# Optimization experiments

Hardware: AMD Instinct MI355X
Metric: run time of the kernel (lower is better)

Reference implementation:

```python
import jax, jax.numpy as jnp
import numpy as np

L, B, CIN, H, W = 32, 4, 3, 16, 16
D, HEADS, DK, DEPTH = 64, 4, 16, 2
EPS = 1e-5
BN_INV = float(1.0 / np.sqrt(1.0 + EPS))  # eval-mode BatchNorm with default stats/affine


def conv2d(x, w, b=None, pad=1, groups=1):
    y = jax.lax.conv_general_dilated(
        x, w, window_strides=(1, 1), padding=[(pad, pad), (pad, pad)],
        dimension_numbers=('NCHW', 'OIHW', 'NCHW'), feature_group_count=groups)
    if b is not None:
        y = y + b[None, :, None, None]
    return y


def layer_norm(x, w, b):
    # LayerNorm over last 3 dims [D,H,W] of (L,B,D,H,W)
    mu = jnp.mean(x, axis=(-3, -2, -1), keepdims=True)
    var = jnp.var(x, axis=(-3, -2, -1), keepdims=True)
    return (x - mu) * jax.lax.rsqrt(var + EPS) * w + b


def pos_table():
    pos = jnp.arange(L, dtype=jnp.float32)
    exp = (2.0 * (jnp.arange(D) // 2).astype(jnp.float32)) / D
    angle = pos[:, None] / jnp.power(10000.0, exp)[None, :]  # (L, D)
    # source applies sin to even POSITIONS and cos to odd POSITIONS (table[0::2]=sin)
    tab = jnp.where((jnp.arange(L) % 2 == 0)[:, None], jnp.sin(angle), jnp.cos(angle))
    return tab[:, None, :, None, None]  # (L,1,D,1,1) broadcast over B,H,W


def reference(x, gw1, gb1, gw2, gb2, gw3, gb3, gw4, gb4,
              conv1_w, conv1_b, conv2_w, conv2_b, wq, wk, wv, w0,
              ln1_w, ln1_b, ln2_w, ln2_b, ff_w1, ff_b1, ff_w2, ff_b2):
    lrelu = lambda v: jax.nn.leaky_relu(v, 0.01)
    h = x.reshape(L * B, CIN, H, W)
    for w_, b_ in ((gw1, gb1), (gw2, gb2), (gw3, gb3), (gw4, gb4)):
        h = lrelu(conv2d(h, w_, b_) * BN_INV)
    xlb = h.reshape(L, B, D, H, W) + pos_table()

    for i in range(DEPTH):
        # ---- multi-head conv attention (dec=True) ----
        y = layer_norm(xlb, ln1_w[i], ln1_b[i])
        xa = jnp.transpose(y, (1, 2, 3, 4, 0))  # (B,D,H,W,L)
        # conv1 is a 1x1 conv == pointwise linear over channels, per head
        qkv = jnp.einsum('bchwl,noc->bnohwl', xa, conv1_w[i]) \
            + conv1_b[i][None, :, :, None, None, None]  # (B,HEADS,3D,H,W,L)
        q, k, v = jnp.split(qkv, 3, axis=2)  # each (B,HEADS,D,H,W,L)
        q = jnp.einsum('bnchwl,nck->bnkhwl', q, wq[i])  # (B,HEADS,DK,H,W,L)
        k = jnp.einsum('bnchwl,nck->bnkhwl', k, wk[i])
        v = jnp.einsum('bnchwl,nck->bnkhwl', v, wv[i])

        def head_conv(t):
            # 5x5 conv per head (no bias): conv2(Q_i + K_j) = conv_w(Q)_i + conv_w(K)_j + bias
            z = jnp.transpose(t, (0, 5, 1, 2, 3, 4)).reshape(B * L, HEADS * DK, H, W)
            z = conv2d(z, conv2_w[i].reshape(HEADS * DK, DK, 5, 5), None, pad=2, groups=HEADS)
            return jnp.transpose(z.reshape(B, L, HEADS, DK, H, W), (0, 2, 3, 4, 5, 1))

        cq = head_conv(q)
        ck = head_conv(k)
        logits = cq[..., :, None] + ck[..., None, :] \
            + conv2_b[i][None, :, :, None, None, None, None]  # (B,HEADS,DK,H,W,Lq,Lk)
        a = jax.nn.softmax(logits, axis=-1)
        vout = jnp.einsum('bnkhwij,bnkhwj->bnkhwi', a, v)   # (B,HEADS,DK,H,W,L)
        vcat = vout.reshape(B, D, H, W, L)                  # concat heads on channel dim
        attn = jnp.einsum('bchwl,co->bohwl', vcat, w0[i])
        xlb = xlb + jnp.transpose(attn, (4, 0, 1, 2, 3))

        # ---- feed-forward over the TIME dimension (Linear on L) ----
        y = layer_norm(xlb, ln2_w[i], ln2_b[i])
        xp = jnp.transpose(y, (1, 2, 3, 4, 0))  # (B,D,H,W,L)
        h1 = lrelu(jnp.einsum('bchwl,ml->bchwm', xp, ff_w1[i]) + ff_b1[i])
        ff = jnp.einsum('bchwm,lm->bchwl', h1, ff_w2[i]) + ff_b2[i]
        xlb = xlb + jnp.transpose(ff, (4, 0, 1, 2, 3))
    return xlb


def setup_inputs() -> dict:
    key = jax.random.key(0)
    specs = {
        'x': (L, B, CIN, H, W),
        'gw1': (4, 3, 3, 3), 'gb1': (4,), 'gw2': (6, 4, 3, 3), 'gb2': (6,),
        'gw3': (8, 6, 3, 3), 'gb3': (8,), 'gw4': (64, 8, 3, 3), 'gb4': (64,),
        'conv1_w': (DEPTH, HEADS, 3 * D, D), 'conv1_b': (DEPTH, HEADS, 3 * D),
        'conv2_w': (DEPTH, HEADS, DK, DK, 5, 5), 'conv2_b': (DEPTH, HEADS, DK),
        'wq': (DEPTH, HEADS, D, DK), 'wk': (DEPTH, HEADS, D, DK), 'wv': (DEPTH, HEADS, D, DK),
        'w0': (DEPTH, D, D),
        'ln1_w': (DEPTH, D, H, W), 'ln1_b': (DEPTH, D, H, W),
        'ln2_w': (DEPTH, D, H, W), 'ln2_b': (DEPTH, D, H, W),
        'ff_w1': (DEPTH, 4 * L, L), 'ff_b1': (DEPTH, 4 * L),
        'ff_w2': (DEPTH, L, 4 * L), 'ff_b2': (DEPTH, L),
    }
    out = {}
    for idx, (name, shape) in enumerate(specs.items()):
        g = jax.random.normal(jax.random.fold_in(key, idx), shape, dtype=jnp.float32)
        if name == 'x':
            out[name] = g
        elif name in ('ln1_w', 'ln2_w'):
            out[name] = 1.0 + 0.05 * g
        else:
            out[name] = 0.05 * g
    return out
```

## Files before the change

kernel.cpp:

```cpp
#include <hip/hip_runtime.h>
#include <math.h>

#define LL 32
#define BB 4
#define DD 64
#define NH 4
#define DKK 16
#define BN_INV 0.9999950000374997f

__device__ __forceinline__ float lrelu(float v){ return v > 0.f ? v : 0.01f*v; }

__global__ __launch_bounds__(256) void k_prep(
    const float* __restrict__ c1w, const float* __restrict__ c1b,
    const float* __restrict__ wk,  const float* __restrict__ wv,
    const float* __restrict__ w2,  const float* __restrict__ gw4,
    const float* __restrict__ ffw2,
    float* __restrict__ A, float* __restrict__ bf, float* __restrict__ pos,
    float* __restrict__ wT, float* __restrict__ wT3, float* __restrict__ w2T){
  int blk = blockIdx.x, t = threadIdx.x;
  if(blk < 64){
    int tid = blk*256 + t;
    int k = tid & 15, d = (tid>>4)&63, n=(tid>>10)&3, tt=(tid>>12)&1, i=tid>>13;
    const float* wsel = (tt ? wv : wk) + (i*NH+n)*64*16;
    const float* cw   = c1w + ((i*NH+n)*192 + (tt+1)*64)*64;
    float acc = 0.f;
    for(int c=0;c<64;++c) acc += cw[c*64+d]*wsel[c*16+k];
    A[tid] = acc;
    if(d==0){
      const float* cb = c1b + (i*NH+n)*192 + (tt+1)*64;
      float ba=0.f;
      for(int c=0;c<64;++c) ba += cb[c]*wsel[c*16+k];
      bf[((i*2+tt)*4+n)*16+k] = ba;
    }
  } else if(blk < 72){
    int tid = (blk-64)*256 + t;
    int d = tid & 63, l = tid >> 6;
    float ex = (float)(d>>1) / 32.0f;
    float angle = (float)l * powf(10000.0f, -ex);
    pos[tid] = (l & 1) ? cosf(angle) : sinf(angle);
  } else if(blk < 272){
    int tid = (blk-72)*256 + t;
    int k = tid & 15; int rest = tid >> 4;
    int tap = rest % 25; int rest2 = rest / 25;
    int c = rest2 & 15; int dn = rest2 >> 4;
    wT[tid] = w2[((dn*16 + k)*16 + c)*25 + tap];
  } else if(blk < 290){
    int tid = (blk-272)*256 + t;
    int co = tid & 63, ct = tid >> 6;
    wT3[ct*64 + co] = gw4[co*72 + ct];
  } else {
    int tid = (blk-290)*256 + t;
    int l = tid & 31; int m = (tid>>5)&127; int dep = tid>>12;
    w2T[tid] = ffw2[dep*4096 + l*128 + m];
  }
}

__global__ __launch_bounds__(256) void k_front(const float* __restrict__ x,
    const float* __restrict__ gw1, const float* __restrict__ gb1,
    const float* __restrict__ gw2, const float* __restrict__ gb2,
    const float* __restrict__ gw3, const float* __restrict__ gb3,
    float* __restrict__ out8){
  __shared__ float sh[4212];
  float* T0 = sh; float* T1 = sh + 972; float* T2 = sh + 2268;
  int f = blockIdx.x, t = threadIdx.x;
  int h = t>>4, w = t&15;
  for(int j=t;j<4212;j+=256) sh[j]=0.f;
  __syncthreads();
  for(int ci=0;ci<3;++ci) T0[ci*324 + (h+1)*18 + (w+1)] = x[f*768 + ci*256 + t];
  __syncthreads();
  for(int co=0;co<4;++co){
    float acc = gb1[co];
    for(int ci=0;ci<3;++ci){
      const float* tb = T0 + ci*324 + h*18 + w;
      const float* wb = gw1 + co*27 + ci*9;
      #pragma unroll
      for(int dy=0;dy<3;++dy)
        #pragma unroll
        for(int dx=0;dx<3;++dx) acc += tb[dy*18+dx]*wb[dy*3+dx];
    }
    T1[co*324 + (h+1)*18 + (w+1)] = lrelu(acc*BN_INV);
  }
  __syncthreads();
  for(int co=0;co<6;++co){
    float acc = gb2[co];
    for(int ci=0;ci<4;++ci){
      const float* tb = T1 + ci*324 + h*18 + w;
      const float* wb = gw2 + co*36 + ci*9;
      #pragma unroll
      for(int dy=0;dy<3;++dy)
        #pragma unroll
        for(int dx=0;dx<3;++dx) acc += tb[dy*18+dx]*wb[dy*3+dx];
    }
    T2[co*324 + (h+1)*18 + (w+1)] = lrelu(acc*BN_INV);
  }
  __syncthreads();
  for(int co=0;co<8;++co){
    float acc = gb3[co];
    for(int ci=0;ci<6;++ci){
      const float* tb = T2 + ci*324 + h*18 + w;
      const float* wb = gw3 + co*54 + ci*9;
      #pragma unroll
      for(int dy=0;dy<3;++dy)
        #pragma unroll
        for(int dx=0;dx<3;++dx) acc += tb[dy*18+dx]*wb[dy*3+dx];
    }
    out8[f*2048 + co*256 + t] = lrelu(acc*BN_INV);
  }
}

__global__ __launch_bounds__(256) void k_conv3_l4(const float* __restrict__ in8,
    const float* __restrict__ wT3, const float* __restrict__ gb4,
    const float* __restrict__ pos, float* __restrict__ out){
  __shared__ float tile[8*324];
  __shared__ float wsl[1152];
  int blk = blockIdx.x; int g = blk & 3; int f = blk >> 2;
  int t = threadIdx.x; int h = t>>4, w = t&15;
  for(int j=t;j<2592;j+=256) tile[j]=0.f;
  for(int j=t;j<1152;j+=256){
    int ct = j>>4, c16 = j&15;
    wsl[j] = wT3[ct*64 + g*16 + c16];
  }
  __syncthreads();
  for(int ci=0;ci<8;++ci) tile[ci*324 + (h+1)*18 + (w+1)] = in8[f*2048 + ci*256 + t];
  __syncthreads();
  float acc[16];
  #pragma unroll
  for(int q=0;q<16;++q) acc[q] = gb4[g*16+q];
  for(int ci=0;ci<8;++ci){
    const float* tb = tile + ci*324 + h*18 + w;
    #pragma unroll
    for(int dy=0;dy<3;++dy){
      #pragma unroll
      for(int dx=0;dx<3;++dx){
        float v = tb[dy*18+dx];
        const float* wp = wsl + (ci*9+dy*3+dx)*16;
        float4 wa = *(const float4*)(wp);
        float4 wb = *(const float4*)(wp+4);
        float4 wc = *(const float4*)(wp+8);
        float4 wd = *(const float4*)(wp+12);
        acc[0]+=v*wa.x; acc[1]+=v*wa.y; acc[2]+=v*wa.z; acc[3]+=v*wa.w;
        acc[4]+=v*wb.x; acc[5]+=v*wb.y; acc[6]+=v*wb.z; acc[7]+=v*wb.w;
        acc[8]+=v*wc.x; acc[9]+=v*wc.y; acc[10]+=v*wc.z; acc[11]+=v*wc.w;
        acc[12]+=v*wd.x; acc[13]+=v*wd.y; acc[14]+=v*wd.z; acc[15]+=v*wd.w;
      }
    }
  }
  int l = f >> 2;
  #pragma unroll
  for(int q=0;q<16;++q){
    float r = lrelu(acc[q]*BN_INV) + pos[l*64 + g*16 + q];
    out[f*16384 + (g*16+q)*256 + t] = r;
  }
}

__global__ __launch_bounds__(1024) void k_stats(const float* __restrict__ x,
                                                float* __restrict__ stats){
  int g = blockIdx.x, t = threadIdx.x;
  const float4* xb = (const float4*)(x + g*16384);
  float s=0.f, s2=0.f;
  #pragma unroll
  for(int j=0;j<4;++j){
    float4 v = xb[t + j*1024];
    s  += v.x + v.y + v.z + v.w;
    s2 += v.x*v.x + v.y*v.y + v.z*v.z + v.w*v.w;
  }
  __shared__ float ls[1024], ls2[1024];
  ls[t]=s; ls2[t]=s2; __syncthreads();
  for(int off=512;off>0;off>>=1){
    if(t<off){ ls[t]+=ls[t+off]; ls2[t]+=ls2[t+off]; }
    __syncthreads();
  }
  if(t==0){
    float mu  = ls[0]*(1.0f/16384.f);
    float var = ls2[0]*(1.0f/16384.f) - mu*mu;
    stats[g*2]   = mu;
    stats[g*2+1] = rsqrtf(var + 1e-5f);
  }
}

__global__ __launch_bounds__(256) void k_kv(const float* __restrict__ x,
                     const float* __restrict__ lnw, const float* __restrict__ lnb,
                     const float* __restrict__ stats,
                     const float* __restrict__ A, const float* __restrict__ bf,
                     float* __restrict__ K, float* __restrict__ V, int dep){
  int blk = blockIdx.x;
  int n = blk & 3; int lb = blk >> 2;
  int t = threadIdx.x;
  float mu = stats[lb*2], ri = stats[lb*2+1];
  const float* xb  = x   + lb*16384 + t;
  const float* wbp = lnw + t;
  const float* bbp = lnb + t;
  const float* akb = A + ((dep*2+0)*4+n)*1024;
  const float* avb = A + ((dep*2+1)*4+n)*1024;
  float kacc[16], vacc[16];
  #pragma unroll
  for(int q=0;q<16;++q){
    kacc[q] = bf[((dep*2+0)*4+n)*16+q];
    vacc[q] = bf[((dep*2+1)*4+n)*16+q];
  }
  for(int d=0;d<64;++d){
    float yv = (xb[d*256]-mu)*ri*wbp[d*256] + bbp[d*256];
    const float* ak = akb + d*16;
    const float* av = avb + d*16;
    #pragma unroll
    for(int q=0;q<16;++q){ kacc[q] += yv*ak[q]; vacc[q] += yv*av[q]; }
  }
  int l = lb >> 2, b = lb & 3;
  int base = ((b*32+l)*4+n)*4096 + t;
  #pragma unroll
  for(int q=0;q<16;++q){ K[base + q*256] = kacc[q]; V[base + q*256] = vacc[q]; }
}

__global__ __launch_bounds__(256) void k_conv5(const float* __restrict__ K,
                       const float* __restrict__ wT, float* __restrict__ CK, int dep){
  __shared__ float tile[16*400];
  int blk = blockIdx.x;
  int khalf = blk & 1; int fh = blk >> 1; int n = fh & 3;
  int t = threadIdx.x;
  const float* kb = K + fh*4096;
  for(int j=t;j<6400;j+=256) tile[j]=0.f;
  __syncthreads();
  int h = t>>4, w = t&15;
  for(int c=0;c<16;++c) tile[c*400 + (h+2)*20 + (w+2)] = kb[c*256+t];
  __syncthreads();
  const float* wb = wT + (dep*4+n)*6400 + khalf*8;
  float acc[8] = {0.f,0.f,0.f,0.f,0.f,0.f,0.f,0.f};
  for(int c=0;c<16;++c){
    const float* tb = tile + c*400 + h*20 + w;
    const float* wc = wb + c*400;
    #pragma unroll
    for(int dy=0;dy<5;++dy){
      #pragma unroll
      for(int dx=0;dx<5;++dx){
        float v = tb[dy*20+dx];
        const float* wp = wc + (dy*5+dx)*16;
        float4 wa = *(const float4*)(wp);
        float4 wbv = *(const float4*)(wp+4);
        acc[0]+=v*wa.x; acc[1]+=v*wa.y; acc[2]+=v*wa.z; acc[3]+=v*wa.w;
        acc[4]+=v*wbv.x; acc[5]+=v*wbv.y; acc[6]+=v*wbv.z; acc[7]+=v*wbv.w;
      }
    }
  }
  float* ob = CK + fh*4096 + khalf*8*256;
  #pragma unroll
  for(int q=0;q<8;++q) ob[q*256+t] = acc[q];
}

__global__ void k_soft(const float* __restrict__ CK, const float* __restrict__ V,
                       float* __restrict__ vout){
  int idx = blockIdx.x*256 + threadIdx.x;
  int p = idx&255; int k=(idx>>8)&15; int n=(idx>>12)&3; int b=idx>>14;
  int base = (b*128 + n)*4096 + k*256 + p;
  float e[32]; float m = -1e30f;
  for(int l=0;l<32;++l){ float v = CK[base + l*16384]; e[l]=v; m = fmaxf(m,v); }
  float s = 0.f;
  for(int l=0;l<32;++l){ e[l] = expf(e[l]-m); s += e[l]; }
  float inv = 1.f/s, acc = 0.f;
  for(int l=0;l<32;++l) acc += e[l]*V[base + l*16384];
  vout[((b*4+n)*16+k)*256+p] = acc*inv;
}

__global__ void k_w0res(const float* __restrict__ vout, const float* __restrict__ w0,
                        float* __restrict__ xlb, int dep){
  int idx = blockIdx.x*256 + threadIdx.x;
  int p = idx&255; int o=(idx>>8)&63; int b=idx>>14;
  const float* vb = vout + b*64*256 + p;
  const float* wb = w0 + dep*4096 + o;
  float acc = 0.f;
  for(int c=0;c<64;++c) acc += vb[c*256]*wb[c*64];
  for(int l=0;l<32;++l) xlb[((l*4+b)*64+o)*256 + p] += acc;
}

__global__ __launch_bounds__(256) void k_ff(float* __restrict__ xlb,
                     const float* __restrict__ lnw, const float* __restrict__ lnb,
                     const float* __restrict__ stats,
                     const float* __restrict__ w1, const float* __restrict__ b1,
                     const float* __restrict__ w2T, const float* __restrict__ b2,
                     int dep){
  __shared__ float pfa[4*2048];
  int t = threadIdx.x;
  int lane = t & 63;
  int w = __builtin_amdgcn_readfirstlane(t >> 6);
  int blk = blockIdx.x;
  int elem = blk*64 + lane;
  int b = elem >> 14;
  int e = elem & 16383;
  float lw  = lnw[e];
  float lbv = lnb[e];
  float xv[32], yv[32];
  #pragma unroll
  for(int l=0;l<32;++l) xv[l] = xlb[elem + l*65536];
  #pragma unroll
  for(int l=0;l<32;++l){
    float mu = stats[(l*4+b)*2];
    float ri = stats[(l*4+b)*2+1];
    yv[l] = (xv[l]-mu)*ri*lw + lbv;
  }
  float fa[32];
  if(w==0){
    #pragma unroll
    for(int l=0;l<32;++l) fa[l] = b2[dep*32+l];
  } else {
    #pragma unroll
    for(int l=0;l<32;++l) fa[l] = 0.f;
  }
  const float* w1b  = w1  + dep*4096 + w*1024;
  const float* w2Tb = w2T + dep*4096 + w*1024;
  const float* b1b  = b1  + dep*128  + w*32;
  #pragma unroll 4
  for(int mm=0;mm<32;++mm){
    float s0=0.f,s1=0.f,s2=0.f,s3=0.f;
    #pragma unroll
    for(int l=0;l<32;l+=4){
      s0 += yv[l+0]*w1b[mm*32+l+0];
      s1 += yv[l+1]*w1b[mm*32+l+1];
      s2 += yv[l+2]*w1b[mm*32+l+2];
      s3 += yv[l+3]*w1b[mm*32+l+3];
    }
    float s = lrelu(((s0+s1)+(s2+s3)) + b1b[mm]);
    #pragma unroll
    for(int l=0;l<32;++l) fa[l] += s*w2Tb[mm*32+l];
  }
  #pragma unroll
  for(int l=0;l<32;++l) pfa[w*2048 + l*64 + lane] = fa[l];
  __syncthreads();
  #pragma unroll
  for(int j=0;j<8;++j){
    int pi = t + j*256;
    float sum = pfa[pi] + pfa[pi+2048] + pfa[pi+4096] + pfa[pi+6144];
    int l = pi >> 6;
    xlb[blk*64 + lane + l*65536] = xv[l] + sum;
  }
}

extern "C" void kernel_launch(void* const* d_in, const int* in_sizes, int n_in,
                              void* d_out, int out_size, void* d_ws, size_t ws_size,
                              hipStream_t stream) {
  const float* x       = (const float*)d_in[0];
  const float* gw1     = (const float*)d_in[1];
  const float* gb1     = (const float*)d_in[2];
  const float* gw2     = (const float*)d_in[3];
  const float* gb2     = (const float*)d_in[4];
  const float* gw3     = (const float*)d_in[5];
  const float* gb3     = (const float*)d_in[6];
  const float* gw4     = (const float*)d_in[7];
  const float* gb4     = (const float*)d_in[8];
  const float* conv1_w = (const float*)d_in[9];
  const float* conv1_b = (const float*)d_in[10];
  const float* conv2_w = (const float*)d_in[11];
  const float* wk      = (const float*)d_in[14];
  const float* wv      = (const float*)d_in[15];
  const float* w0      = (const float*)d_in[16];
  const float* ln1_w   = (const float*)d_in[17];
  const float* ln1_b   = (const float*)d_in[18];
  const float* ln2_w   = (const float*)d_in[19];
  const float* ln2_b   = (const float*)d_in[20];
  const float* ff_w1   = (const float*)d_in[21];
  const float* ff_b1   = (const float*)d_in[22];
  const float* ff_w2   = (const float*)d_in[23];
  const float* ff_b2   = (const float*)d_in[24];

  float* out = (float*)d_out;
  float* ws  = (float*)d_ws;
  float* K     = ws;
  float* CK    = ws + 2097152;
  float* V     = ws + 4194304;
  float* vout  = ws + 6291456;
  float* A     = ws + 6356992;
  float* bf    = ws + 6373376;
  float* pos   = ws + 6373632;
  float* wT    = ws + 6375680;
  float* wT3   = ws + 6426880;
  float* w2T   = ws + 6431488;
  float* stats = ws + 6439680;

  k_prep<<<322, 256, 0, stream>>>(conv1_w, conv1_b, wk, wv, conv2_w, gw4, ff_w2,
                                  A, bf, pos, wT, wT3, w2T);

  k_front   <<<128, 256, 0, stream>>>(x, gw1, gb1, gw2, gb2, gw3, gb3, K);
  k_conv3_l4<<<512, 256, 0, stream>>>(K, wT3, gb4, pos, out);

  for(int dep=0; dep<2; ++dep){
    k_stats<<<128, 1024, 0, stream>>>(out, stats);
    k_kv   <<<512,  256, 0, stream>>>(out, ln1_w + dep*16384, ln1_b + dep*16384,
                                      stats, A, bf, K, V, dep);
    k_conv5<<<1024, 256, 0, stream>>>(K, wT, CK, dep);
    k_soft <<<256,  256, 0, stream>>>(CK, V, vout);
    k_w0res<<<256,  256, 0, stream>>>(vout, w0, out, dep);
    k_stats<<<128, 1024, 0, stream>>>(out, stats);
    k_ff   <<<1024, 256, 0, stream>>>(out, ln2_w + dep*16384, ln2_b + dep*16384,
                                      stats, ff_w1, ff_b1, w2T, ff_b2, dep);
  }
}
```

Baseline: 319.2 us.

## Fuse LayerNorm stats into producer epilogues and merge K/V projection with conv5

Removes the separate k_stats reduction kernels. Each kernel that writes the residual stream now accumulates per-frame sum and sum-of-squares with wave shuffles and atomics into zeroed stat buffers. Consumers derive mean and rsqrt from those sums. The K/V projection kernel also writes K straight into shared memory and runs the 5x5 conv there, dropping the K round-trip through global memory and one launch, at the cost of atomic contention, single-pass variance precision, and fewer conv blocks per frame.

```diff
diff --git a/kernel.cpp b/kernel.cpp
--- a/kernel.cpp
+++ b/kernel.cpp
@@ -10,13 +10,20 @@
 
 __device__ __forceinline__ float lrelu(float v){ return v > 0.f ? v : 0.01f*v; }
 
+__device__ __forceinline__ float wave_sum(float v){
+  #pragma unroll
+  for(int off=1; off<64; off<<=1) v += __shfl_xor(v, off, 64);
+  return v;
+}
+
 __global__ __launch_bounds__(256) void k_prep(
     const float* __restrict__ c1w, const float* __restrict__ c1b,
     const float* __restrict__ wk,  const float* __restrict__ wv,
     const float* __restrict__ w2,  const float* __restrict__ gw4,
     const float* __restrict__ ffw2,
     float* __restrict__ A, float* __restrict__ bf, float* __restrict__ pos,
-    float* __restrict__ wT, float* __restrict__ wT3, float* __restrict__ w2T){
+    float* __restrict__ wT, float* __restrict__ wT3, float* __restrict__ w2T,
+    float* __restrict__ stats){
   int blk = blockIdx.x, t = threadIdx.x;
   if(blk < 64){
     int tid = blk*256 + t;
@@ -48,10 +55,13 @@
     int tid = (blk-272)*256 + t;
     int co = tid & 63, ct = tid >> 6;
     wT3[ct*64 + co] = gw4[co*72 + ct];
-  } else {
+  } else if(blk < 322){
     int tid = (blk-290)*256 + t;
     int l = tid & 31; int m = (tid>>5)&127; int dep = tid>>12;
     w2T[tid] = ffw2[dep*4096 + l*128 + m];
+  } else {
+    #pragma unroll
+    for(int j=0;j<4;++j) stats[t + j*256] = 0.f;
   }
 }
 
@@ -110,7 +120,8 @@
 
 __global__ __launch_bounds__(256) void k_conv3_l4(const float* __restrict__ in8,
     const float* __restrict__ wT3, const float* __restrict__ gb4,
-    const float* __restrict__ pos, float* __restrict__ out){
+    const float* __restrict__ pos, float* __restrict__ out,
+    float* __restrict__ nst){
   __shared__ float tile[8*324];
   __shared__ float wsl[1152];
   int blk = blockIdx.x; int g = blk & 3; int f = blk >> 2;
@@ -146,47 +157,34 @@
     }
   }
   int l = f >> 2;
+  float s = 0.f, s2 = 0.f;
   #pragma unroll
   for(int q=0;q<16;++q){
     float r = lrelu(acc[q]*BN_INV) + pos[l*64 + g*16 + q];
     out[f*16384 + (g*16+q)*256 + t] = r;
-  }
-}
-
-__global__ __launch_bounds__(1024) void k_stats(const float* __restrict__ x,
-                                                float* __restrict__ stats){
-  int g = blockIdx.x, t = threadIdx.x;
-  const float4* xb = (const float4*)(x + g*16384);
-  float s=0.f, s2=0.f;
-  #pragma unroll
-  for(int j=0;j<4;++j){
-    float4 v = xb[t + j*1024];
-    s  += v.x + v.y + v.z + v.w;
-    s2 += v.x*v.x + v.y*v.y + v.z*v.z + v.w*v.w;
-  }
-  __shared__ float ls[1024], ls2[1024];
-  ls[t]=s; ls2[t]=s2; __syncthreads();
-  for(int off=512;off>0;off>>=1){
-    if(t<off){ ls[t]+=ls[t+off]; ls2[t]+=ls2[t+off]; }
-    __syncthreads();
-  }
-  if(t==0){
-    float mu  = ls[0]*(1.0f/16384.f);
-    float var = ls2[0]*(1.0f/16384.f) - mu*mu;
-    stats[g*2]   = mu;
-    stats[g*2+1] = rsqrtf(var + 1e-5f);
-  }
-}
-
-__global__ __launch_bounds__(256) void k_kv(const float* __restrict__ x,
-                     const float* __restrict__ lnw, const float* __restrict__ lnb,
-                     const float* __restrict__ stats,
-                     const float* __restrict__ A, const float* __restrict__ bf,
-                     float* __restrict__ K, float* __restrict__ V, int dep){
+    s += r; s2 += r*r;
+  }
+  float ws_ = wave_sum(s), ws2 = wave_sum(s2);
+  if((t & 63) == 0){
+    atomicAdd(&nst[f*2],   ws_);
+    atomicAdd(&nst[f*2+1], ws2);
+  }
+}
+
+__global__ __launch_bounds__(256) void k_kvc5(const float* __restrict__ x,
+     const float* __restrict__ lnw, const float* __restrict__ lnb,
+     const float* __restrict__ st,
+     const float* __restrict__ A, const float* __restrict__ bf,
+     const float* __restrict__ wT,
+     float* __restrict__ V, float* __restrict__ CK, int dep){
+  __shared__ float tile[16*400];
   int blk = blockIdx.x;
   int n = blk & 3; int lb = blk >> 2;
-  int t = threadIdx.x;
-  float mu = stats[lb*2], ri = stats[lb*2+1];
+  int t = threadIdx.x; int h = t>>4, w = t&15;
+  for(int j=t;j<6400;j+=256) tile[j]=0.f;
+  float Ssum = st[lb*2], S2 = st[lb*2+1];
+  float mu = Ssum*(1.0f/16384.f);
+  float ri = rsqrtf(S2*(1.0f/16384.f) - mu*mu + 1e-5f);
   const float* xb  = x   + lb*16384 + t;
   const float* wbp = lnw + t;
   const float* bbp = lnb + t;
@@ -206,25 +204,18 @@
     for(int q=0;q<16;++q){ kacc[q] += yv*ak[q]; vacc[q] += yv*av[q]; }
   }
   int l = lb >> 2, b = lb & 3;
-  int base = ((b*32+l)*4+n)*4096 + t;
-  #pragma unroll
-  for(int q=0;q<16;++q){ K[base + q*256] = kacc[q]; V[base + q*256] = vacc[q]; }
-}
-
-__global__ __launch_bounds__(256) void k_conv5(const float* __restrict__ K,
-                       const float* __restrict__ wT, float* __restrict__ CK, int dep){
-  __shared__ float tile[16*400];
-  int blk = blockIdx.x;
-  int khalf = blk & 1; int fh = blk >> 1; int n = fh & 3;
-  int t = threadIdx.x;
-  const float* kb = K + fh*4096;
-  for(int j=t;j<6400;j+=256) tile[j]=0.f;
-  __syncthreads();
-  int h = t>>4, w = t&15;
-  for(int c=0;c<16;++c) tile[c*400 + (h+2)*20 + (w+2)] = kb[c*256+t];
-  __syncthreads();
-  const float* wb = wT + (dep*4+n)*6400 + khalf*8;
-  float acc[8] = {0.f,0.f,0.f,0.f,0.f,0.f,0.f,0.f};
+  int fh = (b*32+l)*4+n;
+  __syncthreads();
+  #pragma unroll
+  for(int q=0;q<16;++q){
+    V[fh*4096 + q*256 + t] = vacc[q];
+    tile[q*400 + (h+2)*20 + (w+2)] = kacc[q];
+  }
+  __syncthreads();
+  const float* wb = wT + (dep*4+n)*6400;
+  float acc[16];
+  #pragma unroll
+  for(int q=0;q<16;++q) acc[q] = 0.f;
   for(int c=0;c<16;++c){
     const float* tb = tile + c*400 + h*20 + w;
     const float* wc = wb + c*400;
@@ -236,14 +227,18 @@
         const float* wp = wc + (dy*5+dx)*16;
         float4 wa = *(const float4*)(wp);
         float4 wbv = *(const float4*)(wp+4);
-        acc[0]+=v*wa.x; acc[1]+=v*wa.y; acc[2]+=v*wa.z; acc[3]+=v*wa.w;
+        float4 wcv = *(const float4*)(wp+8);
+        float4 wdv = *(const float4*)(wp+12);
+        acc[0]+=v*wa.x;  acc[1]+=v*wa.y;  acc[2]+=v*wa.z;  acc[3]+=v*wa.w;
         acc[4]+=v*wbv.x; acc[5]+=v*wbv.y; acc[6]+=v*wbv.z; acc[7]+=v*wbv.w;
+        acc[8]+=v*wcv.x; acc[9]+=v*wcv.y; acc[10]+=v*wcv.z; acc[11]+=v*wcv.w;
+        acc[12]+=v*wdv.x; acc[13]+=v*wdv.y; acc[14]+=v*wdv.z; acc[15]+=v*wdv.w;
       }
     }
   }
-  float* ob = CK + fh*4096 + khalf*8*256;
-  #pragma unroll
-  for(int q=0;q<8;++q) ob[q*256+t] = acc[q];
+  float* ob = CK + fh*4096;
+  #pragma unroll
+  for(int q=0;q<16;++q) ob[q*256+t] = acc[q];
 }
 
 __global__ void k_soft(const float* __restrict__ CK, const float* __restrict__ V,
@@ -261,29 +256,38 @@
 }
 
 __global__ void k_w0res(const float* __restrict__ vout, const float* __restrict__ w0,
-                        float* __restrict__ xlb, int dep){
-  int idx = blockIdx.x*256 + threadIdx.x;
-  int p = idx&255; int o=(idx>>8)&63; int b=idx>>14;
+                        float* __restrict__ xlb, float* __restrict__ nst, int dep){
+  int blk = blockIdx.x; int t = threadIdx.x;
+  int p = t; int o = blk & 63; int b = blk >> 6;
   const float* vb = vout + b*64*256 + p;
   const float* wb = w0 + dep*4096 + o;
   float acc = 0.f;
   for(int c=0;c<64;++c) acc += vb[c*256]*wb[c*64];
-  for(int l=0;l<32;++l) xlb[((l*4+b)*64+o)*256 + p] += acc;
+  for(int l=0;l<32;++l){
+    int ix = ((l*4+b)*64+o)*256 + p;
+    float xn = xlb[ix] + acc;
+    xlb[ix] = xn;
+    float s = wave_sum(xn), s2 = wave_sum(xn*xn);
+    if((t & 63) == 0){
+      atomicAdd(&nst[(l*4+b)*2],   s);
+      atomicAdd(&nst[(l*4+b)*2+1], s2);
+    }
+  }
 }
 
 __global__ __launch_bounds__(256) void k_ff(float* __restrict__ xlb,
                      const float* __restrict__ lnw, const float* __restrict__ lnb,
-                     const float* __restrict__ stats,
+                     const float* __restrict__ st,
                      const float* __restrict__ w1, const float* __restrict__ b1,
                      const float* __restrict__ w2T, const float* __restrict__ b2,
-                     int dep){
+                     float* __restrict__ nst, int dep){
   __shared__ float pfa[4*2048];
   int t = threadIdx.x;
   int lane = t & 63;
   int w = __builtin_amdgcn_readfirstlane(t >> 6);
   int blk = blockIdx.x;
   int elem = blk*64 + lane;
-  int b = elem >> 14;
+  int b = blk >> 8;
   int e = elem & 16383;
   float lw  = lnw[e];
   float lbv = lnb[e];
@@ -292,8 +296,9 @@
   for(int l=0;l<32;++l) xv[l] = xlb[elem + l*65536];
   #pragma unroll
   for(int l=0;l<32;++l){
-    float mu = stats[(l*4+b)*2];
-    float ri = stats[(l*4+b)*2+1];
+    float mu = st[(l*4+b)*2]*(1.0f/16384.f);
+    float vv = st[(l*4+b)*2+1]*(1.0f/16384.f) - mu*mu;
+    float ri = rsqrtf(vv + 1e-5f);
     yv[l] = (xv[l]-mu)*ri*lw + lbv;
   }
   float fa[32];
@@ -325,11 +330,20 @@
   for(int l=0;l<32;++l) pfa[w*2048 + l*64 + lane] = fa[l];
   __syncthreads();
   #pragma unroll
-  for(int j=0;j<8;++j){
-    int pi = t + j*256;
-    float sum = pfa[pi] + pfa[pi+2048] + pfa[pi+4096] + pfa[pi+6144];
-    int l = pi >> 6;
-    xlb[blk*64 + lane + l*65536] = xv[l] + sum;
+  for(int l=0;l<32;++l){
+    if((l & 3) == w){
+      int pi = l*64 + lane;
+      float sum = pfa[pi] + pfa[pi+2048] + pfa[pi+4096] + pfa[pi+6144];
+      float xn = xv[l] + sum;
+      xlb[blk*64 + lane + l*65536] = xn;
+      if(nst){
+        float s = wave_sum(xn), s2 = wave_sum(xn*xn);
+        if(lane == 0){
+          atomicAdd(&nst[(l*4+b)*2],   s);
+          atomicAdd(&nst[(l*4+b)*2+1], s2);
+        }
+      }
+    }
   }
 }
 
@@ -362,33 +376,37 @@
 
   float* out = (float*)d_out;
   float* ws  = (float*)d_ws;
-  float* K     = ws;
-  float* CK    = ws + 2097152;
-  float* V     = ws + 4194304;
-  float* vout  = ws + 6291456;
-  float* A     = ws + 6356992;
-  float* bf    = ws + 6373376;
-  float* pos   = ws + 6373632;
-  float* wT    = ws + 6375680;
-  float* wT3   = ws + 6426880;
-  float* w2T   = ws + 6431488;
-  float* stats = ws + 6439680;
-
-  k_prep<<<322, 256, 0, stream>>>(conv1_w, conv1_b, wk, wv, conv2_w, gw4, ff_w2,
-                                  A, bf, pos, wT, wT3, w2T);
-
-  k_front   <<<128, 256, 0, stream>>>(x, gw1, gb1, gw2, gb2, gw3, gb3, K);
-  k_conv3_l4<<<512, 256, 0, stream>>>(K, wT3, gb4, pos, out);
+  float* CK    = ws;
+  float* V     = ws + 2097152;
+  float* vout  = ws + 4194304;
+  float* A     = ws + 4259840;
+  float* bf    = ws + 4276224;
+  float* pos   = ws + 4276480;
+  float* wT    = ws + 4278528;
+  float* wT3   = ws + 4329728;
+  float* w2T   = ws + 4334336;
+  float* stats = ws + 4342528;
+
+  float* st0 = stats;
+  float* st1 = stats + 256;
+  float* st2 = stats + 512;
+  float* st3 = stats + 768;
+
+  k_prep<<<323, 256, 0, stream>>>(conv1_w, conv1_b, wk, wv, conv2_w, gw4, ff_w2,
+                                  A, bf, pos, wT, wT3, w2T, stats);
+
+  k_front   <<<128, 256, 0, stream>>>(x, gw1, gb1, gw2, gb2, gw3, gb3, CK);
+  k_conv3_l4<<<512, 256, 0, stream>>>(CK, wT3, gb4, pos, out, st0);
 
   for(int dep=0; dep<2; ++dep){
-    k_stats<<<128, 1024, 0, stream>>>(out, stats);
-    k_kv   <<<512,  256, 0, stream>>>(out, ln1_w + dep*16384, ln1_b + dep*16384,
-                                      stats, A, bf, K, V, dep);
-    k_conv5<<<1024, 256, 0, stream>>>(K, wT, CK, dep);
+    float* stA = dep ? st2 : st0;
+    float* stB = dep ? st3 : st1;
+    float* stC = dep ? nullptr : st2;
+    k_kvc5 <<<512,  256, 0, stream>>>(out, ln1_w + dep*16384, ln1_b + dep*16384,
+                                      stA, A, bf, wT, V, CK, dep);
     k_soft <<<256,  256, 0, stream>>>(CK, V, vout);
-    k_w0res<<<256,  256, 0, stream>>>(vout, w0, out, dep);
-    k_stats<<<128, 1024, 0, stream>>>(out, stats);
+    k_w0res<<<256,  256, 0, stream>>>(vout, w0, out, stB, dep);
     k_ff   <<<1024, 256, 0, stream>>>(out, ln2_w + dep*16384, ln2_b + dep*16384,
-                                      stats, ff_w1, ff_b1, w2T, ff_b2, dep);
-  }
-}
+                                      stB, ff_w1, ff_b1, w2T, ff_b2, stC, dep);
+  }
+}
```

New measurement: 843.3 us. 2.64x slower.
